# Performance work log

Measured on AMD Instinct MI355X. Metric: run time of the kernel, lower is better.

Reference implementation:

```python
import jax, jax.numpy as jnp
import numpy as np

PATCH_SIZE = 8  # ps
H = W = 512


def _extract_patches(images, ys, xs):
    """images: [B,C,H,W]; ys,xs: [B,N] int patch origins -> [B,N,C,ps,ps]."""
    C = images.shape[1]

    def one_patch(img, y, x):  # img: [C,H,W]
        return jax.lax.dynamic_slice(img, (0, y, x), (C, PATCH_SIZE, PATCH_SIZE))

    per_image = jax.vmap(lambda img, y, x: jax.vmap(one_patch, in_axes=(None, 0, 0))(img, y, x))
    return per_image(images, ys, xs)


def _patch_stats(patches):
    """patches: [B,N,C,ps,ps] -> (mean, unbiased var), each [B,N]."""
    B, N = patches.shape[:2]
    flat = patches.reshape(B, N, -1)
    n = flat.shape[-1]
    mean = flat.mean(axis=-1)
    # torch .var() default is unbiased (divisor n-1)
    var = ((flat - mean[..., None]) ** 2).sum(axis=-1) / (n - 1)
    return mean, var


def setup_inputs() -> dict:
    key = jax.random.key(0)
    kg, kt, k1, k2, k3, k4 = jax.random.split(key, 6)
    B, C = 32, 3
    hi = H - PATCH_SIZE + 1  # 505
    N = 64
    return {
        "generated": jax.random.normal(kg, (B, C, H, W), dtype=jnp.float32),
        "target": jax.random.normal(kt, (B, C, H, W), dtype=jnp.float32),
        "y_gen": jax.random.randint(k1, (B, N), 0, hi, dtype=jnp.int32),
        "x_gen": jax.random.randint(k2, (B, N), 0, hi, dtype=jnp.int32),
        "y_tgt": jax.random.randint(k3, (B, N), 0, hi, dtype=jnp.int32),
        "x_tgt": jax.random.randint(k4, (B, N), 0, hi, dtype=jnp.int32),
    }


def reference(generated, target, y_gen, x_gen, y_tgt, x_tgt):
    gen_patches = _extract_patches(generated, y_gen, x_gen)
    tgt_patches = _extract_patches(target, y_tgt, x_tgt)
    gm, gv = _patch_stats(gen_patches)
    tm, tv = _patch_stats(tgt_patches)
    mean_loss = ((gm - tm) ** 2).mean()
    var_loss = ((gv - tv) ** 2).mean()
    return mean_loss + var_loss
```

## Files before the change

kernel.cpp:

```cpp
#include <hip/hip_runtime.h>

#define IMG_W 512
#define IMG_HW (512 * 512)
#define IMG_CHW (3 * 512 * 512)

__global__ __launch_bounds__(256) void patch_stats_kernel(
    const float* __restrict__ gen, const float* __restrict__ tgt,
    const int* __restrict__ y_gen, const int* __restrict__ x_gen,
    const int* __restrict__ y_tgt, const int* __restrict__ x_tgt,
    float* __restrict__ ws)
{
    const int wave  = threadIdx.x >> 6;
    const int lane  = threadIdx.x & 63;
    const int patch = blockIdx.x * 4 + wave;
    const int b     = patch >> 6;

    const int yg = y_gen[patch], xg = x_gen[patch];
    const int yt = y_tgt[patch], xt = x_tgt[patch];

    const float* __restrict__ gbase = gen + (size_t)b * IMG_CHW;
    const float* __restrict__ tbase = tgt + (size_t)b * IMG_CHW;

    float gv[3], tv[3];
    #pragma unroll
    for (int k = 0; k < 3; ++k) {
        const int e   = lane + 64 * k;
        const int c   = e >> 6;
        const int r   = (e >> 3) & 7;
        const int col = e & 7;
        gv[k] = gbase[c * IMG_HW + (yg + r) * IMG_W + xg + col];
        tv[k] = tbase[c * IMG_HW + (yt + r) * IMG_W + xt + col];
    }

    float gs = gv[0] + gv[1] + gv[2];
    float ts = tv[0] + tv[1] + tv[2];
    #pragma unroll
    for (int off = 32; off; off >>= 1) {
        gs += __shfl_xor(gs, off, 64);
        ts += __shfl_xor(ts, off, 64);
    }
    const float gmean = gs * (1.0f / 192.0f);
    const float tmean = ts * (1.0f / 192.0f);

    float gss = 0.0f, tss = 0.0f;
    #pragma unroll
    for (int k = 0; k < 3; ++k) {
        const float dg = gv[k] - gmean; gss += dg * dg;
        const float dt = tv[k] - tmean; tss += dt * dt;
    }
    #pragma unroll
    for (int off = 32; off; off >>= 1) {
        gss += __shfl_xor(gss, off, 64);
        tss += __shfl_xor(tss, off, 64);
    }

    if (lane == 0) {
        const float gvar = gss * (1.0f / 191.0f);
        const float tvar = tss * (1.0f / 191.0f);
        const float dm = gmean - tmean;
        const float dv = gvar - tvar;
        ws[patch] = dm * dm + dv * dv;
    }
}

__global__ __launch_bounds__(256) void final_reduce_kernel(
    const float* __restrict__ ws, float* __restrict__ out)
{
    float s = 0.0f;
    #pragma unroll
    for (int k = 0; k < 8; ++k) s += ws[threadIdx.x + 256 * k];
    #pragma unroll
    for (int off = 32; off; off >>= 1) s += __shfl_xor(s, off, 64);

    __shared__ float partial[4];
    if ((threadIdx.x & 63) == 0) partial[threadIdx.x >> 6] = s;
    __syncthreads();
    if (threadIdx.x == 0) {
        const float t = partial[0] + partial[1] + partial[2] + partial[3];
        out[0] = t * (1.0f / 2048.0f);
    }
}

extern "C" void kernel_launch(void* const* d_in, const int* in_sizes, int n_in,
                              void* d_out, int out_size, void* d_ws, size_t ws_size,
                              hipStream_t stream) {
    const float* gen = (const float*)d_in[0];
    const float* tgt = (const float*)d_in[1];
    const int*   yg  = (const int*)d_in[2];
    const int*   xg  = (const int*)d_in[3];
    const int*   yt  = (const int*)d_in[4];
    const int*   xt  = (const int*)d_in[5];
    float* out = (float*)d_out;
    float* ws  = (float*)d_ws;

    patch_stats_kernel<<<512, 256, 0, stream>>>(gen, tgt, yg, xg, yt, xt, ws);
    final_reduce_kernel<<<1, 256, 0, stream>>>(ws, out);
}
```

Baseline: 11.33 us.

## Fuse final reduction into patch kernel via per-block flags, single-pass variance

Merges the two kernels into one launch. Each block writes a partial sum and a release flag, and block 0 spins on all 512 flags before reducing them and writing the output. Variance now comes from sum and sum of squares in a single shuffle pass instead of two reduction passes. This removes a kernel launch and a dependency gap, but block 0 busy-waits, which depends on all blocks being co-resident or scheduled eventually. The single-pass formula is also less numerically stable.

```diff
diff --git a/kernel.cpp b/kernel.cpp
--- a/kernel.cpp
+++ b/kernel.cpp
@@ -3,12 +3,15 @@
 #define IMG_W 512
 #define IMG_HW (512 * 512)
 #define IMG_CHW (3 * 512 * 512)
+#define NBLK 512
+#define FLAG_MAGIC 0x5A17D00D
 
-__global__ __launch_bounds__(256) void patch_stats_kernel(
+__global__ __launch_bounds__(256) void tex_loss_fused_kernel(
     const float* __restrict__ gen, const float* __restrict__ tgt,
     const int* __restrict__ y_gen, const int* __restrict__ x_gen,
     const int* __restrict__ y_tgt, const int* __restrict__ x_tgt,
-    float* __restrict__ ws)
+    float* __restrict__ out, float* __restrict__ partials,
+    int* __restrict__ flags)
 {
     const int wave  = threadIdx.x >> 6;
     const int lane  = threadIdx.x & 63;
@@ -32,53 +35,61 @@
         tv[k] = tbase[c * IMG_HW + (yt + r) * IMG_W + xt + col];
     }
 
-    float gs = gv[0] + gv[1] + gv[2];
-    float ts = tv[0] + tv[1] + tv[2];
+    float gs  = gv[0] + gv[1] + gv[2];
+    float ts  = tv[0] + tv[1] + tv[2];
+    float gss = gv[0]*gv[0] + gv[1]*gv[1] + gv[2]*gv[2];
+    float tss = tv[0]*tv[0] + tv[1]*tv[1] + tv[2]*tv[2];
     #pragma unroll
     for (int off = 32; off; off >>= 1) {
-        gs += __shfl_xor(gs, off, 64);
-        ts += __shfl_xor(ts, off, 64);
-    }
-    const float gmean = gs * (1.0f / 192.0f);
-    const float tmean = ts * (1.0f / 192.0f);
-
-    float gss = 0.0f, tss = 0.0f;
-    #pragma unroll
-    for (int k = 0; k < 3; ++k) {
-        const float dg = gv[k] - gmean; gss += dg * dg;
-        const float dt = tv[k] - tmean; tss += dt * dt;
-    }
-    #pragma unroll
-    for (int off = 32; off; off >>= 1) {
+        gs  += __shfl_xor(gs,  off, 64);
+        ts  += __shfl_xor(ts,  off, 64);
         gss += __shfl_xor(gss, off, 64);
         tss += __shfl_xor(tss, off, 64);
     }
 
+    __shared__ float red[4];
     if (lane == 0) {
-        const float gvar = gss * (1.0f / 191.0f);
-        const float tvar = tss * (1.0f / 191.0f);
+        const float gmean = gs * (1.0f / 192.0f);
+        const float tmean = ts * (1.0f / 192.0f);
+        const float gvar = (gss - 192.0f * gmean * gmean) * (1.0f / 191.0f);
+        const float tvar = (tss - 192.0f * tmean * tmean) * (1.0f / 191.0f);
         const float dm = gmean - tmean;
         const float dv = gvar - tvar;
-        ws[patch] = dm * dm + dv * dv;
+        red[wave] = dm * dm + dv * dv;
     }
-}
+    __syncthreads();
 
-__global__ __launch_bounds__(256) void final_reduce_kernel(
-    const float* __restrict__ ws, float* __restrict__ out)
-{
+    if (threadIdx.x == 0) {
+        const float p = red[0] + red[1] + red[2] + red[3];
+        __hip_atomic_store(&partials[blockIdx.x], p,
+                           __ATOMIC_RELAXED, __HIP_MEMORY_SCOPE_AGENT);
+        __hip_atomic_store(&flags[blockIdx.x], FLAG_MAGIC,
+                           __ATOMIC_RELEASE, __HIP_MEMORY_SCOPE_AGENT);
+    }
+
+    if (blockIdx.x != 0) return;
+
+    const int t = threadIdx.x;
     float s = 0.0f;
     #pragma unroll
-    for (int k = 0; k < 8; ++k) s += ws[threadIdx.x + 256 * k];
+    for (int f0 = 0; f0 < NBLK; f0 += 256) {
+        const int f = f0 + t;
+        while (__hip_atomic_load(&flags[f], __ATOMIC_ACQUIRE,
+                                 __HIP_MEMORY_SCOPE_AGENT) != FLAG_MAGIC)
+            __builtin_amdgcn_s_sleep(1);
+        s += __hip_atomic_load(&partials[f], __ATOMIC_RELAXED,
+                               __HIP_MEMORY_SCOPE_AGENT);
+        __hip_atomic_store(&flags[f], 0,
+                           __ATOMIC_RELAXED, __HIP_MEMORY_SCOPE_AGENT);
+    }
     #pragma unroll
     for (int off = 32; off; off >>= 1) s += __shfl_xor(s, off, 64);
 
-    __shared__ float partial[4];
-    if ((threadIdx.x & 63) == 0) partial[threadIdx.x >> 6] = s;
     __syncthreads();
-    if (threadIdx.x == 0) {
-        const float t = partial[0] + partial[1] + partial[2] + partial[3];
-        out[0] = t * (1.0f / 2048.0f);
-    }
+    if (lane == 0) red[wave] = s;
+    __syncthreads();
+    if (t == 0)
+        out[0] = (red[0] + red[1] + red[2] + red[3]) * (1.0f / 2048.0f);
 }
 
 extern "C" void kernel_launch(void* const* d_in, const int* in_sizes, int n_in,
@@ -90,9 +101,10 @@
     const int*   xg  = (const int*)d_in[3];
     const int*   yt  = (const int*)d_in[4];
     const int*   xt  = (const int*)d_in[5];
-    float* out = (float*)d_out;
-    float* ws  = (float*)d_ws;
+    float* out      = (float*)d_out;
+    float* partials = (float*)d_ws;
+    int*   flags    = (int*)((char*)d_ws + NBLK * sizeof(float));
 
-    patch_stats_kernel<<<512, 256, 0, stream>>>(gen, tgt, yg, xg, yt, xt, ws);
-    final_reduce_kernel<<<1, 256, 0, stream>>>(ws, out);
+    tex_loss_fused_kernel<<<NBLK, 256, 0, stream>>>(
+        gen, tgt, yg, xg, yt, xt, out, partials, flags);
 }
```

Result: slower. 13.45 us (+18.7%).
